# Performance work log

Hardware: AMD Instinct MI355X
Metric: run time of the kernel (lower is better)

The kernel has to match this reference:

```python
import jax, jax.numpy as jnp
import numpy as np

N = 4096


def setup_inputs() -> dict:
    key = jax.random.key(0)
    ks = jax.random.split(key, 5)
    s = 1.0 / np.sqrt(N)  # PyTorch Linear default init scale
    return {
        "outer": jax.random.normal(ks[0], (N, N), dtype=jnp.float32),
        "W_slice": jax.random.uniform(ks[1], (N, N), jnp.float32, -s, s),
        "b_slice": jax.random.uniform(ks[2], (N,), jnp.float32, -s, s),
        "W_q": jax.random.uniform(ks[3], (N, N), jnp.float32, -s, s),
        "b_q": jax.random.uniform(ks[4], (N,), jnp.float32, -s, s),
    }


def reference(outer, W_slice, b_slice, W_q, b_q):
    # k = sigmoid(Linear(outer)) then transposed: [n, n] -> [n, n]
    k = jax.nn.sigmoid(outer @ W_slice.T + b_slice).T
    # q = sigmoid(Linear(outer)): [n, n]
    q = jax.nn.sigmoid(outer @ W_q.T + b_q)
    # elementwise score, softmax over last dim (legacy nn.Softmax dim=1 for 2D)
    attn = jax.nn.softmax(q * k, axis=1)
    # weighted sum then reduce: [n, n] @ [n, n] -> [n, n] -> sum(-1) -> [n]
    out = (attn @ outer).sum(-1)
    return out
```

## Files before the change

### kernel.cpp

```cpp
#include <hip/hip_runtime.h>
#include <hip/hip_bf16.h>
#include <hip/hip_fp16.h>

#define NN 4096

typedef __attribute__((ext_vector_type(8))) __bf16 bf16x8;
typedef __attribute__((ext_vector_type(4))) float f32x4;
typedef __attribute__((ext_vector_type(8))) _Float16 f16x8;

static __device__ __forceinline__ unsigned short f2bf_bits(float x) {
  __hip_bfloat16 h = __float2bfloat16(x);
  return __builtin_bit_cast(unsigned short, h);
}

__global__ __launch_bounds__(256) void cast_rowsum_kernel(
    const float* __restrict__ in, __hip_bfloat16* __restrict__ ob,
    float* __restrict__ s) {
  const int row = blockIdx.x;
  const int t = threadIdx.x;
  const float4* rp = (const float4*)(in + (size_t)row * NN);
  unsigned short* op = (unsigned short*)(ob + (size_t)row * NN);
  float sum = 0.f;
#pragma unroll
  for (int it = 0; it < 4; ++it) {
    const int idx = it * 256 + t;
    float4 v = rp[idx];
    sum += (v.x + v.y) + (v.z + v.w);
    ushort4 b;
    b.x = f2bf_bits(v.x);
    b.y = f2bf_bits(v.y);
    b.z = f2bf_bits(v.z);
    b.w = f2bf_bits(v.w);
    *(ushort4*)(op + idx * 4) = b;
  }
#pragma unroll
  for (int o = 32; o > 0; o >>= 1) sum += __shfl_xor(sum, o);
  __shared__ float r[4];
  if ((t & 63) == 0) r[t >> 6] = sum;
  __syncthreads();
  if (t == 0) s[row] = (r[0] + r[1]) + (r[2] + r[3]);
}

__global__ __launch_bounds__(256) void cast_kernel(
    const float* __restrict__ in, __hip_bfloat16* __restrict__ ob) {
  const size_t idx = ((size_t)blockIdx.x * 256 + threadIdx.x) * 4;
  float4 v = *(const float4*)(in + idx);
  ushort4 b;
  b.x = f2bf_bits(v.x);
  b.y = f2bf_bits(v.y);
  b.z = f2bf_bits(v.z);
  b.w = f2bf_bits(v.w);
  *(ushort4*)((unsigned short*)ob + idx) = b;
}

#define BAR() asm volatile("s_barrier" ::: "memory")
#define VMW(N) asm volatile("s_waitcnt vmcnt(" #N ")" ::: "memory")
#define MFMA_(a, b, c) __builtin_amdgcn_mfma_f32_16x16x32_bf16((a), (b), (c), 0, 0, 0)
#define NOOP ((void)0)

#define STAGE_A(dbuf, g, ktE)                                                  \
  do {                                                                         \
    const int r0_ = wm * 128 + (g) * 32 + (wid & 3) * 8;                       \
    __builtin_amdgcn_global_load_lds(                                          \
        (const __attribute__((address_space(1))) void*)(Ag +                   \
            ((size_t)r0_ << 12) + (ktE) + lrowoff),                            \
        (__attribute__((address_space(3))) void*)(&As[dbuf][r0_ * 64]), 16, 0, \
        0);                                                                    \
  } while (0)

#define STAGE_B(dbuf, q, ktE)                                                  \
  do {                                                                         \
    const int r0_ = (q) * 64 + wid * 8;                                        \
    __builtin_amdgcn_global_load_lds(                                          \
        (const __attribute__((address_space(1))) void*)(Bg +                   \
            ((size_t)r0_ << 12) + (ktE) + lrowoff),                            \
        (__attribute__((address_space(3))) void*)(&Bs[dbuf][r0_ * 64]), 16, 0, \
        0);                                                                    \
  } while (0)

#define NOSA(a, b, c) ((void)0)
#define NOSB(a, b, c) ((void)0)

#define LDA8(cb, off) (*(const bf16x8*)((const char*)As[cb] + (off)))
#define LDB8(cb, off) (*(const bf16x8*)((const char*)Bs[cb] + (off)))

#define LOAD_A(cb, g)                                                          \
  af[0] = LDA8(cb, aoff0 + (2 * (g)) * 2048);                                  \
  af[1] = LDA8(cb, aoff1 + (2 * (g)) * 2048);                                  \
  af[2] = LDA8(cb, aoff0 + (2 * (g) + 1) * 2048);                              \
  af[3] = LDA8(cb, aoff1 + (2 * (g) + 1) * 2048);

#define MFMA_PH(g)                                                             \
  __builtin_amdgcn_s_setprio(1);                                               \
  acc[2 * (g)][0] = MFMA_(af[0], bfr[0][0], acc[2 * (g)][0]);                  \
  acc[2 * (g)][1] = MFMA_(af[0], bfr[1][0], acc[2 * (g)][1]);                  \
  acc[2 * (g)][2] = MFMA_(af[0], bfr[2][0], acc[2 * (g)][2]);                  \
  acc[2 * (g)][3] = MFMA_(af[0], bfr[3][0], acc[2 * (g)][3]);                  \
  acc[2 * (g) + 1][0] = MFMA_(af[2], bfr[0][0], acc[2 * (g) + 1][0]);          \
  acc[2 * (g) + 1][1] = MFMA_(af[2], bfr[1][0], acc[2 * (g) + 1][1]);          \
  acc[2 * (g) + 1][2] = MFMA_(af[2], bfr[2][0], acc[2 * (g) + 1][2]);          \
  acc[2 * (g) + 1][3] = MFMA_(af[2], bfr[3][0], acc[2 * (g) + 1][3]);          \
  acc[2 * (g)][0] = MFMA_(af[1], bfr[0][1], acc[2 * (g)][0]);                  \
  acc[2 * (g)][1] = MFMA_(af[1], bfr[1][1], acc[2 * (g)][1]);                  \
  acc[2 * (g)][2] = MFMA_(af[1], bfr[2][1], acc[2 * (g)][2]);                  \
  acc[2 * (g)][3] = MFMA_(af[1], bfr[3][1], acc[2 * (g)][3]);                  \
  acc[2 * (g) + 1][0] = MFMA_(af[3], bfr[0][1], acc[2 * (g) + 1][0]);          \
  acc[2 * (g) + 1][1] = MFMA_(af[3], bfr[1][1], acc[2 * (g) + 1][1]);          \
  acc[2 * (g) + 1][2] = MFMA_(af[3], bfr[2][1], acc[2 * (g) + 1][2]);          \
  acc[2 * (g) + 1][3] = MFMA_(af[3], bfr[3][1], acc[2 * (g) + 1][3]);          \
  __builtin_amdgcn_s_setprio(0);

#define KTILE(cb, kn1, kn2, SA0, SBX, SA3, W)                                  \
  {                                                                            \
    bfr[0][0] = LDB8(cb, boff0 + 0);                                           \
    bfr[0][1] = LDB8(cb, boff1 + 0);                                           \
    bfr[1][0] = LDB8(cb, boff0 + 2048);                                        \
    bfr[1][1] = LDB8(cb, boff1 + 2048);                                        \
    bfr[2][0] = LDB8(cb, boff0 + 4096);                                        \
    bfr[2][1] = LDB8(cb, boff1 + 4096);                                        \
    bfr[3][0] = LDB8(cb, boff0 + 6144);                                        \
    bfr[3][1] = LDB8(cb, boff1 + 6144);                                        \
    LOAD_A(cb, 0);                                                             \
    SA0((cb) ^ 1, 2, kn1);                                                     \
    SA0((cb) ^ 1, 3, kn1);                                                     \
    BAR();                                                                     \
    MFMA_PH(0);                                                                \
    BAR();                                                                     \
    LOAD_A(cb, 1);                                                             \
    SBX(cb, 0, kn2);                                                           \
    SBX(cb, 1, kn2);                                                           \
    BAR();                                                                     \
    MFMA_PH(1);                                                                \
    BAR();                                                                     \
    LOAD_A(cb, 2);                                                             \
    SBX(cb, 2, kn2);                                                           \
    SBX(cb, 3, kn2);                                                           \
    BAR();                                                                     \
    MFMA_PH(2);                                                                \
    BAR();                                                                     \
    LOAD_A(cb, 3);                                                             \
    SA3(cb, 0, kn2);                                                           \
    SA3(cb, 1, kn2);                                                           \
    BAR();                                                                     \
    MFMA_PH(3);                                                                \
    W;                                                                         \
    BAR();                                                                     \
  }

__global__ __launch_bounds__(512, 2) void gemm_sig(
    const unsigned short* __restrict__ A, const unsigned short* __restrict__ B,
    const float* __restrict__ bias, __half* __restrict__ C, int bias_row) {
  __shared__ __align__(128) unsigned short As[2][16384];
  __shared__ __align__(128) unsigned short Bs[2][16384];

  const int tid = threadIdx.x;
  const int wid = tid >> 6;
  const int lane = tid & 63;
  const int wm = wid >> 2;
  const int wn = wid & 3;

  const int bid = blockIdx.x;
  const int xcd = bid & 7;
  const int idx = bid >> 3;
  const int brow = ((xcd >> 1) * 4 + (idx >> 3)) * 256;
  const int bcol = ((xcd & 1) * 8 + (idx & 7)) * 256;

  const unsigned short* Ag = A + (size_t)brow * NN;
  const unsigned short* Bg = B + (size_t)bcol * NN;

  const size_t lrowoff = (size_t)(lane >> 3) * NN + (((lane & 7) ^ (lane >> 3)) * 8);

  const int fr = lane & 15;
  const int frlow = lane & 7;
  const int quad = lane >> 4;
  const int aoff0 = (wm * 128 + fr) * 128 + (((quad) ^ frlow) << 4);
  const int aoff1 = (wm * 128 + fr) * 128 + (((quad + 4) ^ frlow) << 4);
  const int boff0 = (wn * 64 + fr) * 128 + (((quad) ^ frlow) << 4);
  const int boff1 = (wn * 64 + fr) * 128 + (((quad + 4) ^ frlow) << 4);

  f32x4 acc[8][4];
#pragma unroll
  for (int m = 0; m < 8; ++m)
#pragma unroll
    for (int n = 0; n < 4; ++n) acc[m][n] = (f32x4){0.f, 0.f, 0.f, 0.f};

  bf16x8 bfr[4][2], af[4];

  STAGE_B(0, 0, 0);
  STAGE_B(0, 1, 0);
  STAGE_B(0, 2, 0);
  STAGE_B(0, 3, 0);
  STAGE_A(0, 0, 0);
  STAGE_A(0, 1, 0);
  STAGE_A(0, 2, 0);
  STAGE_A(0, 3, 0);
  STAGE_B(1, 0, 64);
  STAGE_B(1, 1, 64);
  STAGE_B(1, 2, 64);
  STAGE_B(1, 3, 64);
  STAGE_A(1, 0, 64);
  STAGE_A(1, 1, 64);
  VMW(6);
  BAR();

  int kt = 0;
  for (int it = 0; it < 31; ++it) {
    KTILE(0, kt + 64, kt + 128, STAGE_A, STAGE_B, STAGE_A, VMW(6));
    KTILE(1, kt + 128, kt + 192, STAGE_A, STAGE_B, STAGE_A, VMW(6));
    kt += 128;
  }
  KTILE(0, 4032, 0, STAGE_A, NOSB, NOSA, VMW(0));
  KTILE(1, 0, 0, NOSA, NOSB, NOSA, NOOP);

  const int cr0 = (lane >> 4) * 4;
  const int cc = lane & 15;
#pragma unroll
  for (int m = 0; m < 8; ++m) {
#pragma unroll
    for (int n = 0; n < 4; ++n) {
#pragma unroll
      for (int j = 0; j < 4; ++j) {
        const int gi = brow + wm * 128 + m * 16 + cr0 + j;
        const int gj = bcol + wn * 64 + n * 16 + cc;
        float v = acc[m][n][j] + (bias_row ? bias[gi] : bias[gj]);
        C[(size_t)gi * NN + gj] = __float2half(1.0f / (1.0f + __expf(-v)));
      }
    }
  }
}

__global__ __launch_bounds__(256) void softmax_out_kernel(
    const __half* __restrict__ q, const __half* __restrict__ k,
    const float* __restrict__ s, float* __restrict__ out) {
  const int i = blockIdx.x;
  const int t = threadIdx.x;
  const __half* qr = q + (size_t)i * NN;
  const __half* kr = k + (size_t)i * NN;
  float se = 0.f, ses = 0.f;
#pragma unroll
  for (int it = 0; it < 2; ++it) {
    const int j0 = (it * 256 + t) * 8;
    f16x8 qv = *(const f16x8*)(qr + j0);
    f16x8 kv = *(const f16x8*)(kr + j0);
    float4 s0 = *(const float4*)(s + j0);
    float4 s1 = *(const float4*)(s + j0 + 4);
    float sj[8] = {s0.x, s0.y, s0.z, s0.w, s1.x, s1.y, s1.z, s1.w};
#pragma unroll
    for (int u = 0; u < 8; ++u) {
      float sc = (float)qv[u] * (float)kv[u];
      float e = __expf(sc);
      se += e;
      ses += e * sj[u];
    }
  }
#pragma unroll
  for (int o = 32; o > 0; o >>= 1) {
    se += __shfl_xor(se, o);
    ses += __shfl_xor(ses, o);
  }
  __shared__ float r1[4], r2[4];
  if ((t & 63) == 0) {
    r1[t >> 6] = se;
    r2[t >> 6] = ses;
  }
  __syncthreads();
  if (t == 0)
    out[i] = ((r2[0] + r2[1]) + (r2[2] + r2[3])) /
             ((r1[0] + r1[1]) + (r1[2] + r1[3]));
}

extern "C" void kernel_launch(void* const* d_in, const int* in_sizes, int n_in,
                              void* d_out, int out_size, void* d_ws,
                              size_t ws_size, hipStream_t stream) {
  const float* outer = (const float*)d_in[0];
  const float* W_slice = (const float*)d_in[1];
  const float* b_slice = (const float*)d_in[2];
  const float* W_q = (const float*)d_in[3];
  const float* b_q = (const float*)d_in[4];
  float* out = (float*)d_out;

  char* ws = (char*)d_ws;
  const size_t MSZ = (size_t)NN * NN * 2;
  __hip_bfloat16* outer_bf = (__hip_bfloat16*)(ws);
  __hip_bfloat16* wsl_bf = (__hip_bfloat16*)(ws + MSZ);
  __hip_bfloat16* wq_bf = (__hip_bfloat16*)(ws + 2 * MSZ);
  __half* qh = (__half*)(ws + 3 * MSZ);
  __half* kh = (__half*)(ws + 4 * MSZ);
  float* s = (float*)(ws + 5 * MSZ);

  cast_rowsum_kernel<<<NN, 256, 0, stream>>>(outer, outer_bf, s);
  cast_kernel<<<NN * NN / 1024, 256, 0, stream>>>(W_slice, wsl_bf);
  cast_kernel<<<NN * NN / 1024, 256, 0, stream>>>(W_q, wq_bf);

  gemm_sig<<<256, 512, 0, stream>>>((const unsigned short*)outer_bf,
                                    (const unsigned short*)wq_bf, b_q, qh, 0);
  gemm_sig<<<256, 512, 0, stream>>>((const unsigned short*)wsl_bf,
                                    (const unsigned short*)outer_bf, b_slice,
                                    kh, 1);

  softmax_out_kernel<<<NN, 256, 0, stream>>>(qh, kh, s, out);
}
```

Baseline: 460.2 us.

## Switch GEMM to 32x32x16 MFMA, halve barriers, merge both GEMMs into one launch

Replaces the 16x16x32 bf16 MFMA tiling with 32x32x16 MFMAs, which need fewer LDS fragment reads per FLOP. The k-tile schedule is restructured to use one barrier per phase instead of two, double-buffering A fragments. The q and k GEMMs now run as a single 512-block launch that selects operands by block index, filling the GPU with both workloads at once. The risks are higher register pressure from 16-wide accumulators, the epilogue writing with a less favourable pattern, and possible LDS races from the reduced barriers.

```diff
diff --git a/kernel.cpp b/kernel.cpp
--- a/kernel.cpp
+++ b/kernel.cpp
@@ -6,6 +6,7 @@
 
 typedef __attribute__((ext_vector_type(8))) __bf16 bf16x8;
 typedef __attribute__((ext_vector_type(4))) float f32x4;
+typedef __attribute__((ext_vector_type(16))) float f32x16;
 typedef __attribute__((ext_vector_type(8))) _Float16 f16x8;
 
 static __device__ __forceinline__ unsigned short f2bf_bits(float x) {
@@ -55,7 +56,7 @@
 
 #define BAR() asm volatile("s_barrier" ::: "memory")
 #define VMW(N) asm volatile("s_waitcnt vmcnt(" #N ")" ::: "memory")
-#define MFMA_(a, b, c) __builtin_amdgcn_mfma_f32_16x16x32_bf16((a), (b), (c), 0, 0, 0)
+#define MF32(a, b, c) __builtin_amdgcn_mfma_f32_32x32x16_bf16((a), (b), (c), 0, 0, 0)
 #define NOOP ((void)0)
 
 #define STAGE_A(dbuf, g, ktE)                                                  \
@@ -84,72 +85,65 @@
 #define LDA8(cb, off) (*(const bf16x8*)((const char*)As[cb] + (off)))
 #define LDB8(cb, off) (*(const bf16x8*)((const char*)Bs[cb] + (off)))
 
-#define LOAD_A(cb, g)                                                          \
-  af[0] = LDA8(cb, aoff0 + (2 * (g)) * 2048);                                  \
-  af[1] = LDA8(cb, aoff1 + (2 * (g)) * 2048);                                  \
-  af[2] = LDA8(cb, aoff0 + (2 * (g) + 1) * 2048);                              \
-  af[3] = LDA8(cb, aoff1 + (2 * (g) + 1) * 2048);
-
-#define MFMA_PH(g)                                                             \
+#define LOAD_A32(cb, g, bk)                                                    \
+  af[bk][0] = LDA8(cb, aBase + (g)*4096 + ak0);                                \
+  af[bk][1] = LDA8(cb, aBase + (g)*4096 + ak1);                                \
+  af[bk][2] = LDA8(cb, aBase + (g)*4096 + ak2);                                \
+  af[bk][3] = LDA8(cb, aBase + (g)*4096 + ak3);
+
+#define LOAD_B32(cb)                                                           \
+  bfr[0][0] = LDB8(cb, bBase + ak0);                                           \
+  bfr[0][1] = LDB8(cb, bBase + ak1);                                           \
+  bfr[0][2] = LDB8(cb, bBase + ak2);                                           \
+  bfr[0][3] = LDB8(cb, bBase + ak3);                                           \
+  bfr[1][0] = LDB8(cb, bBase + 4096 + ak0);                                    \
+  bfr[1][1] = LDB8(cb, bBase + 4096 + ak1);                                    \
+  bfr[1][2] = LDB8(cb, bBase + 4096 + ak2);                                    \
+  bfr[1][3] = LDB8(cb, bBase + 4096 + ak3);
+
+#define MFMA_PH32(g, bk)                                                       \
   __builtin_amdgcn_s_setprio(1);                                               \
-  acc[2 * (g)][0] = MFMA_(af[0], bfr[0][0], acc[2 * (g)][0]);                  \
-  acc[2 * (g)][1] = MFMA_(af[0], bfr[1][0], acc[2 * (g)][1]);                  \
-  acc[2 * (g)][2] = MFMA_(af[0], bfr[2][0], acc[2 * (g)][2]);                  \
-  acc[2 * (g)][3] = MFMA_(af[0], bfr[3][0], acc[2 * (g)][3]);                  \
-  acc[2 * (g) + 1][0] = MFMA_(af[2], bfr[0][0], acc[2 * (g) + 1][0]);          \
-  acc[2 * (g) + 1][1] = MFMA_(af[2], bfr[1][0], acc[2 * (g) + 1][1]);          \
-  acc[2 * (g) + 1][2] = MFMA_(af[2], bfr[2][0], acc[2 * (g) + 1][2]);          \
-  acc[2 * (g) + 1][3] = MFMA_(af[2], bfr[3][0], acc[2 * (g) + 1][3]);          \
-  acc[2 * (g)][0] = MFMA_(af[1], bfr[0][1], acc[2 * (g)][0]);                  \
-  acc[2 * (g)][1] = MFMA_(af[1], bfr[1][1], acc[2 * (g)][1]);                  \
-  acc[2 * (g)][2] = MFMA_(af[1], bfr[2][1], acc[2 * (g)][2]);                  \
-  acc[2 * (g)][3] = MFMA_(af[1], bfr[3][1], acc[2 * (g)][3]);                  \
-  acc[2 * (g) + 1][0] = MFMA_(af[3], bfr[0][1], acc[2 * (g) + 1][0]);          \
-  acc[2 * (g) + 1][1] = MFMA_(af[3], bfr[1][1], acc[2 * (g) + 1][1]);          \
-  acc[2 * (g) + 1][2] = MFMA_(af[3], bfr[2][1], acc[2 * (g) + 1][2]);          \
-  acc[2 * (g) + 1][3] = MFMA_(af[3], bfr[3][1], acc[2 * (g) + 1][3]);          \
+  acc[g][0] = MF32(af[bk][0], bfr[0][0], acc[g][0]);                           \
+  acc[g][1] = MF32(af[bk][0], bfr[1][0], acc[g][1]);                           \
+  acc[g][0] = MF32(af[bk][1], bfr[0][1], acc[g][0]);                           \
+  acc[g][1] = MF32(af[bk][1], bfr[1][1], acc[g][1]);                           \
+  acc[g][0] = MF32(af[bk][2], bfr[0][2], acc[g][0]);                           \
+  acc[g][1] = MF32(af[bk][2], bfr[1][2], acc[g][1]);                           \
+  acc[g][0] = MF32(af[bk][3], bfr[0][3], acc[g][0]);                           \
+  acc[g][1] = MF32(af[bk][3], bfr[1][3], acc[g][1]);                           \
   __builtin_amdgcn_s_setprio(0);
 
-#define KTILE(cb, kn1, kn2, SA0, SBX, SA3, W)                                  \
+#define KTILE32(cb, kn1, kn2, SA0, SBX, SA3, W)                                \
   {                                                                            \
-    bfr[0][0] = LDB8(cb, boff0 + 0);                                           \
-    bfr[0][1] = LDB8(cb, boff1 + 0);                                           \
-    bfr[1][0] = LDB8(cb, boff0 + 2048);                                        \
-    bfr[1][1] = LDB8(cb, boff1 + 2048);                                        \
-    bfr[2][0] = LDB8(cb, boff0 + 4096);                                        \
-    bfr[2][1] = LDB8(cb, boff1 + 4096);                                        \
-    bfr[3][0] = LDB8(cb, boff0 + 6144);                                        \
-    bfr[3][1] = LDB8(cb, boff1 + 6144);                                        \
-    LOAD_A(cb, 0);                                                             \
+    LOAD_B32(cb);                                                              \
+    LOAD_A32(cb, 0, 0);                                                        \
+    LOAD_A32(cb, 1, 1);                                                        \
     SA0((cb) ^ 1, 2, kn1);                                                     \
     SA0((cb) ^ 1, 3, kn1);                                                     \
+    MFMA_PH32(0, 0);                                                           \
     BAR();                                                                     \
-    MFMA_PH(0);                                                                \
-    BAR();                                                                     \
-    LOAD_A(cb, 1);                                                             \
+    LOAD_A32(cb, 2, 0);                                                        \
     SBX(cb, 0, kn2);                                                           \
     SBX(cb, 1, kn2);                                                           \
+    MFMA_PH32(1, 1);                                                           \
     BAR();                                                                     \
-    MFMA_PH(1);                                                                \
-    BAR();                                                                     \
-    LOAD_A(cb, 2);                                                             \
+    LOAD_A32(cb, 3, 1);                                                        \
     SBX(cb, 2, kn2);                                                           \
     SBX(cb, 3, kn2);                                                           \
+    MFMA_PH32(2, 0);                                                           \
     BAR();                                                                     \
-    MFMA_PH(2);                                                                \
-    BAR();                                                                     \
-    LOAD_A(cb, 3);                                                             \
     SA3(cb, 0, kn2);                                                           \
     SA3(cb, 1, kn2);                                                           \
-    BAR();                                                                     \
-    MFMA_PH(3);                                                                \
+    MFMA_PH32(3, 1);                                                           \
     W;                                                                         \
     BAR();                                                                     \
   }
 
 __global__ __launch_bounds__(512, 2) void gemm_sig(
-    const unsigned short* __restrict__ A, const unsigned short* __restrict__ B,
-    const float* __restrict__ bias, __half* __restrict__ C, int bias_row) {
+    const unsigned short* __restrict__ Aq, const unsigned short* __restrict__ Bq,
+    const unsigned short* __restrict__ Ak, const unsigned short* __restrict__ Bk,
+    const float* __restrict__ bias_q, const float* __restrict__ bias_k,
+    __half* __restrict__ Cq, __half* __restrict__ Ck) {
   __shared__ __align__(128) unsigned short As[2][16384];
   __shared__ __align__(128) unsigned short Bs[2][16384];
 
@@ -159,7 +153,14 @@
   const int wm = wid >> 2;
   const int wn = wid & 3;
 
-  const int bid = blockIdx.x;
+  const int sel = blockIdx.x >> 8;
+  const unsigned short* __restrict__ A = sel ? Ak : Aq;
+  const unsigned short* __restrict__ B = sel ? Bk : Bq;
+  const float* __restrict__ bias = sel ? bias_k : bias_q;
+  __half* __restrict__ C = sel ? Ck : Cq;
+  const int bias_row = sel;
+
+  const int bid = blockIdx.x & 255;
   const int xcd = bid & 7;
   const int idx = bid >> 3;
   const int brow = ((xcd >> 1) * 4 + (idx >> 3)) * 256;
@@ -168,23 +169,28 @@
   const unsigned short* Ag = A + (size_t)brow * NN;
   const unsigned short* Bg = B + (size_t)bcol * NN;
 
-  const size_t lrowoff = (size_t)(lane >> 3) * NN + (((lane & 7) ^ (lane >> 3)) * 8);
-
-  const int fr = lane & 15;
-  const int frlow = lane & 7;
-  const int quad = lane >> 4;
-  const int aoff0 = (wm * 128 + fr) * 128 + (((quad) ^ frlow) << 4);
-  const int aoff1 = (wm * 128 + fr) * 128 + (((quad + 4) ^ frlow) << 4);
-  const int boff0 = (wn * 64 + fr) * 128 + (((quad) ^ frlow) << 4);
-  const int boff1 = (wn * 64 + fr) * 128 + (((quad + 4) ^ frlow) << 4);
-
-  f32x4 acc[8][4];
-#pragma unroll
-  for (int m = 0; m < 8; ++m)
-#pragma unroll
-    for (int n = 0; n < 4; ++n) acc[m][n] = (f32x4){0.f, 0.f, 0.f, 0.f};
-
-  bf16x8 bfr[4][2], af[4];
+  const size_t lrowoff =
+      (size_t)(lane >> 3) * NN + (((lane & 7) ^ (lane >> 3)) * 8);
+
+  const int l31 = lane & 31;
+  const int l7 = lane & 7;
+  const int hi = lane >> 5;
+  const int aBase = (wm * 128 + l31) * 128;
+  const int bBase = (wn * 64 + l31) * 128;
+  const int ak0 = ((0 + hi) ^ l7) << 4;
+  const int ak1 = ((2 + hi) ^ l7) << 4;
+  const int ak2 = ((4 + hi) ^ l7) << 4;
+  const int ak3 = ((6 + hi) ^ l7) << 4;
+
+  f32x16 acc[4][2];
+#pragma unroll
+  for (int m = 0; m < 4; ++m)
+#pragma unroll
+    for (int n = 0; n < 2; ++n)
+#pragma unroll
+      for (int j = 0; j < 16; ++j) acc[m][n][j] = 0.f;
+
+  bf16x8 bfr[2][4], af[2][4];
 
   STAGE_B(0, 0, 0);
   STAGE_B(0, 1, 0);
@@ -205,24 +211,22 @@
 
   int kt = 0;
   for (int it = 0; it < 31; ++it) {
-    KTILE(0, kt + 64, kt + 128, STAGE_A, STAGE_B, STAGE_A, VMW(6));
-    KTILE(1, kt + 128, kt + 192, STAGE_A, STAGE_B, STAGE_A, VMW(6));
+    KTILE32(0, kt + 64, kt + 128, STAGE_A, STAGE_B, STAGE_A, VMW(6));
+    KTILE32(1, kt + 128, kt + 192, STAGE_A, STAGE_B, STAGE_A, VMW(6));
     kt += 128;
   }
-  KTILE(0, 4032, 0, STAGE_A, NOSB, NOSA, VMW(0));
-  KTILE(1, 0, 0, NOSA, NOSB, NOSA, NOOP);
-
-  const int cr0 = (lane >> 4) * 4;
-  const int cc = lane & 15;
-#pragma unroll
-  for (int m = 0; m < 8; ++m) {
-#pragma unroll
-    for (int n = 0; n < 4; ++n) {
-#pragma unroll
-      for (int j = 0; j < 4; ++j) {
-        const int gi = brow + wm * 128 + m * 16 + cr0 + j;
-        const int gj = bcol + wn * 64 + n * 16 + cc;
-        float v = acc[m][n][j] + (bias_row ? bias[gi] : bias[gj]);
+  KTILE32(0, 4032, 0, STAGE_A, NOSB, NOSA, VMW(0));
+  KTILE32(1, 0, 0, NOSA, NOSB, NOSA, NOOP);
+
+#pragma unroll
+  for (int mf = 0; mf < 4; ++mf) {
+#pragma unroll
+    for (int nf = 0; nf < 2; ++nf) {
+#pragma unroll
+      for (int j = 0; j < 16; ++j) {
+        const int gi = brow + wm * 128 + mf * 32 + (j & 3) + 8 * (j >> 2) + 4 * hi;
+        const int gj = bcol + wn * 64 + nf * 32 + l31;
+        float v = acc[mf][nf][j] + (bias_row ? bias[gi] : bias[gj]);
         C[(size_t)gi * NN + gj] = __float2half(1.0f / (1.0f + __expf(-v)));
       }
     }
@@ -292,11 +296,10 @@
   cast_kernel<<<NN * NN / 1024, 256, 0, stream>>>(W_slice, wsl_bf);
   cast_kernel<<<NN * NN / 1024, 256, 0, stream>>>(W_q, wq_bf);
 
-  gemm_sig<<<256, 512, 0, stream>>>((const unsigned short*)outer_bf,
-                                    (const unsigned short*)wq_bf, b_q, qh, 0);
-  gemm_sig<<<256, 512, 0, stream>>>((const unsigned short*)wsl_bf,
-                                    (const unsigned short*)outer_bf, b_slice,
-                                    kh, 1);
+  gemm_sig<<<512, 512, 0, stream>>>(
+      (const unsigned short*)outer_bf, (const unsigned short*)wq_bf,
+      (const unsigned short*)wsl_bf, (const unsigned short*)outer_bf, b_q,
+      b_slice, qh, kh);
 
   softmax_out_kernel<<<NN, 256, 0, stream>>>(qh, kh, s, out);
 }
```

New measurement: 484.9 us. 5.4% more time.
